# Kernel optimization log

Hardware: AMD Instinct MI355X
Metric: run time of the kernel (lower is better)

## Reference

```python
import jax, jax.numpy as jnp
import numpy as np

B, S, UC = 64, 5, 50          # batch, sample (candidates), clicked history
D, T = 128, 768               # embedding_size, title_size
NE, NR, NN = 200000, 100, 50000  # entities, relations, news
K, A = 10, 20                 # neighbors per entity, anchor nodes per news


def _lin(k, out_d, in_d):
    w = jax.random.normal(k, (out_d, in_d), jnp.float32) * (1.0 / np.sqrt(in_d))
    b = jnp.zeros((out_d,), jnp.float32)
    return w, b


def setup_inputs() -> dict:
    key = jax.random.key(0)
    ks = jax.random.split(key, 16)
    W_nc1, b_nc1 = _lin(ks[0], D, T)
    W_nc2, b_nc2 = _lin(ks[1], D, D)
    W_anchor, b_anchor = _lin(ks[2], D, 2 * D)
    W_aw1, b_aw1 = _lin(ks[3], D, D)
    W_aw2, b_aw2 = _lin(ks[4], 1, D)
    W_mlp1, b_mlp1 = _lin(ks[5], D, 2 * D)
    W_mlp2, b_mlp2 = _lin(ks[6], D, D)
    return {
        "news_title_embedding": jax.random.normal(ks[7], (NN, T), jnp.float32),
        "entity_embedding": jax.random.normal(ks[8], (NE, D), jnp.float32),
        "relation_embedding": jax.random.normal(ks[9], (NR, D), jnp.float32),
        "W_nc1": W_nc1, "b_nc1": b_nc1, "W_nc2": W_nc2, "b_nc2": b_nc2,
        "W_anchor": W_anchor, "b_anchor": b_anchor,
        "W_aw1": W_aw1, "b_aw1": b_aw1, "W_aw2": W_aw2, "b_aw2": b_aw2,
        "W_mlp1": W_mlp1, "b_mlp1": b_mlp1, "W_mlp2": W_mlp2, "b_mlp2": b_mlp2,
        "cand_news": jax.random.randint(ks[10], (B, S), 0, NN, jnp.int32),
        "clicked_news": jax.random.randint(ks[11], (B, UC), 0, NN, jnp.int32),
        "cand_anchor_nodes": jax.random.randint(ks[12], (B * S, A), 0, NE, jnp.int32),
        "clicked_anchor_nodes": jax.random.randint(ks[13], (B * UC, A), 0, NE, jnp.int32),
        "entity_adj": jax.random.randint(ks[14], (NE, K), 0, NE, jnp.int32),
        "relation_adj": jax.random.randint(ks[15], (NE, K), 0, NR, jnp.int32),
    }


def reference(news_title_embedding, entity_embedding, relation_embedding,
              W_nc1, b_nc1, W_nc2, b_nc2,
              W_anchor, b_anchor, W_aw1, b_aw1, W_aw2, b_aw2,
              W_mlp1, b_mlp1, W_mlp2, b_mlp2,
              cand_news, clicked_news, cand_anchor_nodes, clicked_anchor_nodes,
              entity_adj, relation_adj):
    elu = jax.nn.elu

    def news_emb(ids_flat):  # [N] -> [N, D]
        t = news_title_embedding[ids_flat]                       # [N, T]
        return jnp.tanh(elu(t @ W_nc1.T + b_nc1) @ W_nc2.T + b_nc2)

    def anchor_graph_emb(nodes):  # [N, A] -> [N, D]
        node_e = entity_embedding[nodes]                          # [N, A, D]
        nb_ent = entity_embedding[entity_adj[nodes]]              # [N, A, K, D]
        nb_rel = relation_embedding[relation_adj[nodes]]          # [N, A, K, D]
        agg = jnp.sum(nb_ent + nb_rel, axis=-2)                   # [N, A, D]
        h = jnp.tanh(jnp.concatenate([node_e, agg], axis=-1) @ W_anchor.T + b_anchor)
        logits = elu(h @ W_aw1.T + b_aw1) @ W_aw2.T + b_aw2       # [N, A, 1]
        w = jax.nn.softmax(logits, axis=-2)                       # softmax over anchor nodes
        return jnp.sum(h * w, axis=-2)                            # [N, D]

    cand_e = news_emb(cand_news.reshape(-1))                      # [B*S, D]
    clk_e = news_emb(clicked_news.reshape(-1))                    # [B*UC, D]
    cand_e = jnp.concatenate([cand_e, anchor_graph_emb(cand_anchor_nodes)], axis=-1)
    clk_e = jnp.concatenate([clk_e, anchor_graph_emb(clicked_anchor_nodes)], axis=-1)

    def mlp(x):
        return elu(elu(x @ W_mlp1.T + b_mlp1) @ W_mlp2.T + b_mlp2)

    news_embedding = mlp(cand_e).reshape(B, S, -1)                # [B, S, D]
    user_embedding = jnp.mean(mlp(clk_e).reshape(B, UC, -1), axis=1)  # [B, D]
    score = jnp.sum(news_embedding * user_embedding[:, None, :], axis=-1)  # [B, S]
    return score
```

## Files before the change

kernel.cpp:

```cpp
#include <hip/hip_runtime.h>
#include <hip/hip_bf16.h>


#define B_ 64
#define S_ 5
#define UC_ 50
#define A_ 20
#define NCAND 320
#define NCLK 3200
#define NNEWS 3520
#define NANCH 70400

static constexpr long OFF_WNC1P = 64;
static constexpr long OFF_BNC1  = 98368;
static constexpr long OFF_WNC2P = 98496;
static constexpr long OFF_BNC2  = 114880;
static constexpr long OFF_WANCP = 115008;
static constexpr long OFF_BANC  = 147776;
static constexpr long OFF_WAW1P = 147904;
static constexpr long OFF_BAW1  = 164288;
static constexpr long OFF_WAW2  = 164416;
static constexpr long OFF_BAW2  = 164544;
static constexpr long OFF_WM1P  = 164548;
static constexpr long OFF_BM1   = 197316;
static constexpr long OFF_WM2P  = 197444;
static constexpr long OFF_BM2   = 213828;
static constexpr long OFF_REL   = 213956;
static constexpr long OFF_AE    = 226756;
static constexpr long OFF_NE    = 677316;
static constexpr long OFF_MO    = 1127876;

typedef __attribute__((ext_vector_type(8))) short short8v;
typedef __attribute__((ext_vector_type(4))) float f32x4;

__device__ __forceinline__ float ldf(const void* p, long i, int bf) {
  if (bf) {
    unsigned int u = (unsigned int)((const unsigned short*)p)[i];
    u <<= 16;
    return __uint_as_float(u);
  }
  return ((const float*)p)[i];
}

__device__ __forceinline__ float4 ldf4(const void* p, long i, int bf) {
  float4 f;
  if (bf) {
    const unsigned short* q = (const unsigned short*)p + i;
    uint2 u = *(const uint2*)q;
    f.x = __uint_as_float(u.x << 16);
    f.y = __uint_as_float(u.x & 0xffff0000u);
    f.z = __uint_as_float(u.y << 16);
    f.w = __uint_as_float(u.y & 0xffff0000u);
  } else {
    f = *(const float4*)((const float*)p + i);
  }
  return f;
}

__device__ __forceinline__ float eluf(float v) { return v > 0.f ? v : expm1f(v); }

__device__ __forceinline__ void splitbf(float v, unsigned short& hi, unsigned short& lo) {
  unsigned int b = __float_as_uint(v);
  hi = (unsigned short)(b >> 16);
  float rm = v - __uint_as_float(b & 0xffff0000u);
  unsigned int rb = __float_as_uint(rm);
  lo = (unsigned short)((rb + 0x7fffu + ((rb >> 16) & 1u)) >> 16);
}

__device__ __forceinline__ float bfh(unsigned short u) {
  return __uint_as_float((unsigned int)u << 16);
}

__global__ void k_detect(const void* ent, int* flag) {
  __shared__ int cnt;
  if (threadIdx.x == 0) cnt = 0;
  __syncthreads();
  unsigned short u = ((const unsigned short*)ent)[threadIdx.x];
  int e = (u >> 7) & 0xFF;
  int ok = (e >= 107 && e <= 146) ? 1 : 0;
  atomicAdd(&cnt, ok);
  __syncthreads();
  if (threadIdx.x == 0) *flag = (cnt >= 200) ? 1 : 0;
}

__global__ __launch_bounds__(256) void k_prep(
    const void* s0, const void* s1, const void* s2, const void* s3,
    const void* s4, const void* s5, const void* s6, const void* s7,
    const void* s8, const void* s9, const void* s10, const void* s11,
    const void* s12, const void* s13, const void* s14, float* ws) {
  const int bf = ((const int*)ws)[0];
  const void* srcs[15] = {s0,s1,s2,s3,s4,s5,s6,s7,s8,s9,s10,s11,s12,s13,s14};
  const int R[15] = {128,128,128,128,128,128,128,128,1,  1,  128,128,128,128,100};
  const int C[15] = {768,1,  128,1,  256,1,  128,1,  128,1,  256,1,  128,1,  128};
  const int MD[15]= {2,  0,  2,  0,  3,  0,  3,  0,  0,  0,  2,  0,  2,  0,  0};
  const long OFF[15] = {OFF_WNC1P,OFF_BNC1,OFF_WNC2P,OFF_BNC2,OFF_WANCP,OFF_BANC,
                        OFF_WAW1P,OFF_BAW1,OFF_WAW2,OFF_BAW2,OFF_WM1P,OFF_BM1,
                        OFF_WM2P,OFF_BM2,OFF_REL};
  const long total = 226689;
  for (long idx = (long)blockIdx.x * blockDim.x + threadIdx.x; idx < total;
       idx += (long)gridDim.x * blockDim.x) {
    long rem = idx;
    int s = 0;
    while (rem >= (long)R[s] * C[s]) { rem -= (long)R[s] * C[s]; s++; }
    float v = ldf(srcs[s], rem, bf);
    if (MD[s] == 2) {
      long r = rem / C[s], c = rem - r * C[s];
      ws[OFF[s] + (c >> 2) * 512 + r * 4 + (c & 3)] = v;
    } else if (MD[s] == 3) {
      long r = rem / C[s], c = rem - r * C[s];
      unsigned short hi, lo;
      splitbf(v, hi, lo);
      unsigned short* H = (unsigned short*)(ws + OFF[s]);
      unsigned short* L = H + (s == 4 ? 32768 : 16384);
      long id2 = ((c >> 5) * 128 + r) * 32 + (c & 31);
      H[id2] = hi;
      L[id2] = lo;
    } else {
      ws[OFF[s] + rem] = v;
    }
  }
}

__global__ __launch_bounds__(128) void k_news(const void* titles, const int* cand,
                                              const int* clk, float* ws) {
  const int bf = ((const int*)ws)[0];
  __shared__ __align__(16) float t[8][768];
  __shared__ __align__(16) float h1[8][128];
  int tid = threadIdx.x;
  long r0 = (long)blockIdx.x * 8;
  for (int x = tid * 4; x < 8 * 768; x += 128 * 4) {
    int c = x / 768, k = x - c * 768;
    long i = r0 + c;
    int id = (i < NCAND) ? cand[i] : clk[i - NCAND];
    *(float4*)&t[c][k] = ldf4(titles, (long)id * 768 + k, bf);
  }
  __syncthreads();
  int j = tid;
  const float4* W1 = (const float4*)(ws + OFF_WNC1P);
  float acc[8];
#pragma unroll
  for (int c = 0; c < 8; c++) acc[c] = 0.f;
  for (int k4 = 0; k4 < 192; k4++) {
    float4 w = W1[k4 * 128 + j];
#pragma unroll
    for (int c = 0; c < 8; c++) {
      const float4 xv = *(const float4*)&t[c][k4 * 4];
      acc[c] += w.x * xv.x + w.y * xv.y + w.z * xv.z + w.w * xv.w;
    }
  }
  float b1 = ws[OFF_BNC1 + j];
#pragma unroll
  for (int c = 0; c < 8; c++) h1[c][j] = eluf(acc[c] + b1);
  __syncthreads();
  const float4* W2 = (const float4*)(ws + OFF_WNC2P);
  float a2[8];
#pragma unroll
  for (int c = 0; c < 8; c++) a2[c] = 0.f;
  for (int k4 = 0; k4 < 32; k4++) {
    float4 w = W2[k4 * 128 + j];
#pragma unroll
    for (int c = 0; c < 8; c++) {
      const float4 xv = *(const float4*)&h1[c][k4 * 4];
      a2[c] += w.x * xv.x + w.y * xv.y + w.z * xv.z + w.w * xv.w;
    }
  }
  float b2 = ws[OFF_BNC2 + j];
  float* NE = ws + OFF_NE;
#pragma unroll
  for (int c = 0; c < 8; c++) NE[(r0 + c) * 128 + j] = tanhf(a2[c] + b2);
}

__global__ __launch_bounds__(256, 3) void k_anchor(const void* ent, const int* canda,
                                                   const int* clka, const int* eadj,
                                                   const int* radj, float* ws) {
  __shared__ __align__(16) unsigned short XbH[32][264];
  __shared__ __align__(16) unsigned short XbL[32][264];
  __shared__ __align__(16) unsigned short Hhi[32][136];
  __shared__ __align__(16) unsigned short Hlo[32][136];
  __shared__ int NodeIdL[20];
  __shared__ int EAdjL[200];
  __shared__ int RAdjL[200];
  __shared__ float LGp[4][20];

  const int bf = ((const int*)ws)[0];
  int tid = threadIdx.x;
  int lane = tid & 63, wv = tid >> 6;
  int r16 = lane & 15, khh = lane >> 4;
  int lane32 = tid & 31, grp = tid >> 5;
  const float* relf = ws + OFF_REL;

  const unsigned short* WAH = (const unsigned short*)(ws + OFF_WANCP);
  const unsigned short* WAL = WAH + 32768;
  const unsigned short* W1H = (const unsigned short*)(ws + OFF_WAW1P);
  const unsigned short* W1L = W1H + 16384;

  if (tid < 20) {
    long n = (long)blockIdx.x * 20 + tid;
    NodeIdL[tid] = (n < (long)NCAND * A_) ? canda[n] : clka[n - (long)NCAND * A_];
  }
  __syncthreads();
  if (tid < 200) {
    int rr = tid / 10, kk = tid - rr * 10;
    int nd = NodeIdL[rr];
    EAdjL[tid] = eadj[(long)nd * 10 + kk];
    RAdjL[tid] = radj[(long)nd * 10 + kk];
  }
  __syncthreads();

#pragma unroll
  for (int i = 0; i < 3; ++i) {
    int row = grp + i * 8;
    if (row < 20) {
      int node = NodeIdL[row];
      float4 x1 = ldf4(ent, (long)node * 128 + lane32 * 4, bf);
      float4 a = {0.f, 0.f, 0.f, 0.f};
#pragma unroll
      for (int k = 0; k < 10; ++k) {
        int an = EAdjL[row * 10 + k], rn = RAdjL[row * 10 + k];
        float4 e = ldf4(ent, (long)an * 128 + lane32 * 4, bf);
        const float4 r = *(const float4*)&relf[(long)rn * 128 + lane32 * 4];
        a.x += e.x + r.x;
        a.y += e.y + r.y;
        a.z += e.z + r.z;
        a.w += e.w + r.w;
      }
      ushort4 h4, l4;
      splitbf(x1.x, h4.x, l4.x); splitbf(x1.y, h4.y, l4.y);
      splitbf(x1.z, h4.z, l4.z); splitbf(x1.w, h4.w, l4.w);
      *(ushort4*)&XbH[row][lane32 * 4] = h4;
      *(ushort4*)&XbL[row][lane32 * 4] = l4;
      splitbf(a.x, h4.x, l4.x); splitbf(a.y, h4.y, l4.y);
      splitbf(a.z, h4.z, l4.z); splitbf(a.w, h4.w, l4.w);
      *(ushort4*)&XbH[row][128 + lane32 * 4] = h4;
      *(ushort4*)&XbL[row][128 + lane32 * 4] = l4;
    }
  }
  __syncthreads();

  {
    int n0 = wv * 32 + r16, n1 = n0 + 16;
    f32x4 acc[2][2] = {};
    for (int kt = 0; kt < 8; ++kt) {
      long w0 = ((long)(kt * 128 + n0)) * 32 + khh * 8;
      long w1 = ((long)(kt * 128 + n1)) * 32 + khh * 8;
      short8v b0h = *(const short8v*)(WAH + w0);
      short8v b0l = *(const short8v*)(WAL + w0);
      short8v b1h = *(const short8v*)(WAH + w1);
      short8v b1l = *(const short8v*)(WAL + w1);
#pragma unroll
      for (int mt = 0; mt < 2; ++mt) {
        short8v ahi = *(const short8v*)&XbH[mt * 16 + r16][kt * 32 + khh * 8];
        short8v alo = *(const short8v*)&XbL[mt * 16 + r16][kt * 32 + khh * 8];
        acc[mt][0] = __builtin_amdgcn_mfma_f32_16x16x32_bf16(ahi, b0h, acc[mt][0], 0, 0, 0);
        acc[mt][0] = __builtin_amdgcn_mfma_f32_16x16x32_bf16(ahi, b0l, acc[mt][0], 0, 0, 0);
        acc[mt][0] = __builtin_amdgcn_mfma_f32_16x16x32_bf16(alo, b0h, acc[mt][0], 0, 0, 0);
        acc[mt][1] = __builtin_amdgcn_mfma_f32_16x16x32_bf16(ahi, b1h, acc[mt][1], 0, 0, 0);
        acc[mt][1] = __builtin_amdgcn_mfma_f32_16x16x32_bf16(ahi, b1l, acc[mt][1], 0, 0, 0);
        acc[mt][1] = __builtin_amdgcn_mfma_f32_16x16x32_bf16(alo, b1h, acc[mt][1], 0, 0, 0);
      }
    }
    float bc0 = ws[OFF_BANC + n0], bc1 = ws[OFF_BANC + n1];
#pragma unroll
    for (int mt = 0; mt < 2; ++mt)
#pragma unroll
      for (int j = 0; j < 4; ++j) {
        int r = mt * 16 + khh * 4 + j;
        if (r < 20) {
          unsigned short hi, lo;
          float h0 = tanhf(acc[mt][0][j] + bc0);
          splitbf(h0, hi, lo);
          Hhi[r][n0] = hi; Hlo[r][n0] = lo;
          float h1 = tanhf(acc[mt][1][j] + bc1);
          splitbf(h1, hi, lo);
          Hhi[r][n1] = hi; Hlo[r][n1] = lo;
        }
      }
  }
  __syncthreads();

  {
    int n0 = wv * 32 + r16, n1 = n0 + 16;
    float b10 = ws[OFF_BAW1 + n0], b11 = ws[OFF_BAW1 + n1];
    float w20 = ws[OFF_WAW2 + n0], w21 = ws[OFF_WAW2 + n1];
    f32x4 ac[2][2] = {};
    for (int kt = 0; kt < 4; ++kt) {
      long w0 = ((long)(kt * 128 + n0)) * 32 + khh * 8;
      long w1 = ((long)(kt * 128 + n1)) * 32 + khh * 8;
      short8v b0h = *(const short8v*)(W1H + w0);
      short8v b0l = *(const short8v*)(W1L + w0);
      short8v b1h = *(const short8v*)(W1H + w1);
      short8v b1l = *(const short8v*)(W1L + w1);
#pragma unroll
      for (int mt = 0; mt < 2; ++mt) {
        short8v ahi = *(const short8v*)&Hhi[mt * 16 + r16][kt * 32 + khh * 8];
        short8v alo = *(const short8v*)&Hlo[mt * 16 + r16][kt * 32 + khh * 8];
        ac[mt][0] = __builtin_amdgcn_mfma_f32_16x16x32_bf16(ahi, b0h, ac[mt][0], 0, 0, 0);
        ac[mt][0] = __builtin_amdgcn_mfma_f32_16x16x32_bf16(ahi, b0l, ac[mt][0], 0, 0, 0);
        ac[mt][0] = __builtin_amdgcn_mfma_f32_16x16x32_bf16(alo, b0h, ac[mt][0], 0, 0, 0);
        ac[mt][1] = __builtin_amdgcn_mfma_f32_16x16x32_bf16(ahi, b1h, ac[mt][1], 0, 0, 0);
        ac[mt][1] = __builtin_amdgcn_mfma_f32_16x16x32_bf16(ahi, b1l, ac[mt][1], 0, 0, 0);
        ac[mt][1] = __builtin_amdgcn_mfma_f32_16x16x32_bf16(alo, b1h, ac[mt][1], 0, 0, 0);
      }
    }
#pragma unroll
    for (int mt = 0; mt < 2; ++mt)
#pragma unroll
      for (int j = 0; j < 4; ++j) {
        float v = eluf(ac[mt][0][j] + b10) * w20 + eluf(ac[mt][1][j] + b11) * w21;
        v += __shfl_xor(v, 1);
        v += __shfl_xor(v, 2);
        v += __shfl_xor(v, 4);
        v += __shfl_xor(v, 8);
        int r = mt * 16 + khh * 4 + j;
        if (r16 == 0 && r < 20) LGp[wv][r] = v;
      }
  }
  __syncthreads();

  if (tid < 128) {
    float bw2 = ws[OFF_BAW2];
    float e[20], mx = -1e30f;
#pragma unroll
    for (int a = 0; a < 20; ++a) {
      e[a] = LGp[0][a] + LGp[1][a] + LGp[2][a] + LGp[3][a] + bw2;
      mx = fmaxf(mx, e[a]);
    }
    float s = 0.f;
#pragma unroll
    for (int a = 0; a < 20; ++a) { e[a] = expf(e[a] - mx); s += e[a]; }
    float inv = 1.0f / s;
    float o = 0.f;
#pragma unroll
    for (int a = 0; a < 20; ++a)
      o += e[a] * (bfh(Hhi[a][tid]) + bfh(Hlo[a][tid]));
    float* AE = ws + OFF_AE;
    AE[(long)blockIdx.x * 128 + tid] = o * inv;
  }
}

__global__ __launch_bounds__(256) void k_mlp(float* ws) {
  __shared__ __align__(16) float xt[16][256];
  __shared__ __align__(16) float h1[16][128];
  int tid = threadIdx.x;
  long r0 = (long)blockIdx.x * 16;
  const float* NE = ws + OFF_NE;
  const float* AE = ws + OFF_AE;
  for (int x = tid; x < 16 * 256; x += 256) {
    int c = x >> 8, k = x & 255;
    xt[c][k] = (k < 128) ? NE[(r0 + c) * 128 + k] : AE[(r0 + c) * 128 + (k - 128)];
  }
  __syncthreads();
  int j = tid & 127, half = tid >> 7;
  const float4* W1 = (const float4*)(ws + OFF_WM1P);
  float acc[8];
#pragma unroll
  for (int c = 0; c < 8; c++) acc[c] = 0.f;
  for (int k4 = 0; k4 < 64; k4++) {
    float4 w = W1[k4 * 128 + j];
#pragma unroll
    for (int c = 0; c < 8; c++) {
      const float4 xv = *(const float4*)&xt[half * 8 + c][k4 * 4];
      acc[c] += w.x * xv.x + w.y * xv.y + w.z * xv.z + w.w * xv.w;
    }
  }
  float b1 = ws[OFF_BM1 + j];
#pragma unroll
  for (int c = 0; c < 8; c++) h1[half * 8 + c][j] = eluf(acc[c] + b1);
  __syncthreads();
  const float4* W2 = (const float4*)(ws + OFF_WM2P);
  float a2[8];
#pragma unroll
  for (int c = 0; c < 8; c++) a2[c] = 0.f;
  for (int k4 = 0; k4 < 32; k4++) {
    float4 w = W2[k4 * 128 + j];
#pragma unroll
    for (int c = 0; c < 8; c++) {
      const float4 xv = *(const float4*)&h1[half * 8 + c][k4 * 4];
      a2[c] += w.x * xv.x + w.y * xv.y + w.z * xv.z + w.w * xv.w;
    }
  }
  float b2 = ws[OFF_BM2 + j];
  float* MO = ws + OFF_MO;
#pragma unroll
  for (int c = 0; c < 8; c++) MO[(r0 + half * 8 + c) * 128 + j] = eluf(a2[c] + b2);
}

__global__ __launch_bounds__(128) void k_score(const float* ws, void* out) {
  const int bf = ((const int*)ws)[0];
  int b = blockIdx.x;
  int d = threadIdx.x;
  const float* MO = ws + OFF_MO;
  float u = 0.f;
  for (int t = 0; t < UC_; t++) u += MO[(long)(NCAND + b * UC_ + t) * 128 + d];
  u *= (1.0f / UC_);
  __shared__ float red[2];
  for (int s = 0; s < S_; s++) {
    float p = MO[(long)(b * S_ + s) * 128 + d] * u;
#pragma unroll
    for (int o = 32; o > 0; o >>= 1) p += __shfl_down(p, o, 64);
    if ((d & 63) == 0) red[d >> 6] = p;
    __syncthreads();
    if (d == 0) {
      float v = red[0] + red[1];
      if (bf)
        ((__hip_bfloat16*)out)[b * S_ + s] = __float2bfloat16(v);
      else
        ((float*)out)[b * S_ + s] = v;
    }
    __syncthreads();
  }
}

extern "C" void kernel_launch(void* const* d_in, const int* in_sizes, int n_in,
                              void* d_out, int out_size, void* d_ws, size_t ws_size,
                              hipStream_t stream) {
  (void)in_sizes; (void)n_in; (void)out_size; (void)ws_size;
  const void* titles = d_in[0];
  const void* ent    = d_in[1];
  const void* rel    = d_in[2];
  const void* Wnc1 = d_in[3];  const void* bnc1 = d_in[4];
  const void* Wnc2 = d_in[5];  const void* bnc2 = d_in[6];
  const void* Wanc = d_in[7];  const void* banc = d_in[8];
  const void* Waw1 = d_in[9];  const void* baw1 = d_in[10];
  const void* Waw2 = d_in[11]; const void* baw2 = d_in[12];
  const void* Wm1  = d_in[13]; const void* bm1  = d_in[14];
  const void* Wm2  = d_in[15]; const void* bm2  = d_in[16];
  const int* cand  = (const int*)d_in[17];
  const int* clk   = (const int*)d_in[18];
  const int* canda = (const int*)d_in[19];
  const int* clka  = (const int*)d_in[20];
  const int* eadj  = (const int*)d_in[21];
  const int* radj  = (const int*)d_in[22];
  float* ws = (float*)d_ws;

  k_detect<<<1, 256, 0, stream>>>(ent, (int*)d_ws);
  k_prep<<<256, 256, 0, stream>>>(Wnc1, bnc1, Wnc2, bnc2, Wanc, banc, Waw1, baw1,
                                  Waw2, baw2, Wm1, bm1, Wm2, bm2, rel, ws);
  k_news<<<NNEWS / 8, 128, 0, stream>>>(titles, cand, clk, ws);
  k_anchor<<<NNEWS, 256, 0, stream>>>(ent, canda, clka, eadj, radj, ws);
  k_mlp<<<NNEWS / 16, 256, 0, stream>>>(ws);
  k_score<<<B_, 128, 0, stream>>>(ws, d_out);
}
```

Baseline: 224.2 us.

## Stage bf16 entity gathers via global_load_lds with swizzled LDS and trimmed MFMAs

When entity embeddings are bf16, the node and neighbour rows are gathered straight into LDS with global_load_lds instead of through registers. The node half of the anchor input is exact in bf16, so its low-part MFMAs are skipped. The shared arrays shrink to 20 rows with XOR swizzling to avoid bank conflicts, and the padded rows 20-31 are aliased onto valid rows rather than read. LDS use rises because of the 200-row raw buffer, so the occupancy hint drops from 3 to 2 blocks per CU.

```diff
diff --git a/kernel.cpp b/kernel.cpp
--- a/kernel.cpp
+++ b/kernel.cpp
@@ -33,6 +33,19 @@
 typedef __attribute__((ext_vector_type(8))) short short8v;
 typedef __attribute__((ext_vector_type(4))) float f32x4;
 
+typedef const __attribute__((address_space(1))) void* gas_ptr;
+typedef __attribute__((address_space(3))) void* las_ptr;
+
+__device__ __forceinline__ void gld_lds16(const void* g, void* l) {
+  __builtin_amdgcn_global_load_lds(
+      (gas_ptr)(unsigned long long)g,
+      (las_ptr)(unsigned int)(unsigned long long)l, 16, 0, 0);
+}
+
+__device__ __forceinline__ int swz(int row, int col) {
+  return (((col >> 3) ^ (row & 7)) << 3) | (col & 7);
+}
+
 __device__ __forceinline__ float ldf(const void* p, long i, int bf) {
   if (bf) {
     unsigned int u = (unsigned int)((const unsigned short*)p)[i];
@@ -54,6 +67,15 @@
   } else {
     f = *(const float4*)((const float*)p + i);
   }
+  return f;
+}
+
+__device__ __forceinline__ float4 cvtbf4(uint2 u) {
+  float4 f;
+  f.x = __uint_as_float(u.x << 16);
+  f.y = __uint_as_float(u.x & 0xffff0000u);
+  f.z = __uint_as_float(u.y << 16);
+  f.w = __uint_as_float(u.y & 0xffff0000u);
   return f;
 }
 
@@ -170,17 +192,20 @@
   for (int c = 0; c < 8; c++) NE[(r0 + c) * 128 + j] = tanhf(a2[c] + b2);
 }
 
-__global__ __launch_bounds__(256, 3) void k_anchor(const void* ent, const int* canda,
+__global__ __launch_bounds__(256, 2) void k_anchor(const void* ent, const int* canda,
                                                    const int* clka, const int* eadj,
                                                    const int* radj, float* ws) {
-  __shared__ __align__(16) unsigned short XbH[32][264];
-  __shared__ __align__(16) unsigned short XbL[32][264];
-  __shared__ __align__(16) unsigned short Hhi[32][136];
-  __shared__ __align__(16) unsigned short Hlo[32][136];
+  __shared__ __align__(16) unsigned short AggRaw[200][128];
+  __shared__ __align__(16) unsigned short XbNodeH[20][128];
+  __shared__ __align__(16) unsigned short XbAggH[20][128];
+  __shared__ __align__(16) unsigned short XbAggL[20][128];
+  __shared__ __align__(16) unsigned short Hhi[20][128];
+  __shared__ __align__(16) unsigned short Hlo[20][128];
   __shared__ int NodeIdL[20];
   __shared__ int EAdjL[200];
   __shared__ int RAdjL[200];
   __shared__ float LGp[4][20];
+  unsigned short (*XbNodeL)[128] = (unsigned short(*)[128])&AggRaw[0][0];
 
   const int bf = ((const int*)ws)[0];
   int tid = threadIdx.x;
@@ -207,32 +232,75 @@
   }
   __syncthreads();
 
-#pragma unroll
-  for (int i = 0; i < 3; ++i) {
-    int row = grp + i * 8;
-    if (row < 20) {
-      int node = NodeIdL[row];
-      float4 x1 = ldf4(ent, (long)node * 128 + lane32 * 4, bf);
-      float4 a = {0.f, 0.f, 0.f, 0.f};
+  if (bf) {
+    const char* entb = (const char*)ent;
+    int lq = lane & 15;
+    int rq = lane >> 4;
+    for (int i = wv; i < 55; i += 4) {
+      if (i < 5) {
+        int row4 = i * 4;
+        int id = NodeIdL[row4 + rq];
+        int sg = lq ^ ((row4 + rq) & 7);
+        gld_lds16(entb + (long)id * 256 + sg * 16, &XbNodeH[row4][0]);
+      } else {
+        int row4 = (i - 5) * 4;
+        int id = EAdjL[row4 + rq];
+        gld_lds16(entb + (long)id * 256 + lq * 16, &AggRaw[row4][0]);
+      }
+    }
+  }
+  __syncthreads();
+
+  if (bf) {
+#pragma unroll
+    for (int ii = 0; ii < 3; ++ii) {
+      if (ii == 2 && wv >= 2) break;
+      int a = grp + ii * 8;
+      float4 s = {0.f, 0.f, 0.f, 0.f};
 #pragma unroll
       for (int k = 0; k < 10; ++k) {
-        int an = EAdjL[row * 10 + k], rn = RAdjL[row * 10 + k];
-        float4 e = ldf4(ent, (long)an * 128 + lane32 * 4, bf);
-        const float4 r = *(const float4*)&relf[(long)rn * 128 + lane32 * 4];
-        a.x += e.x + r.x;
-        a.y += e.y + r.y;
-        a.z += e.z + r.z;
-        a.w += e.w + r.w;
+        float4 e = cvtbf4(*(const uint2*)&AggRaw[a * 10 + k][lane32 * 4]);
+        const float4 r = *(const float4*)&relf[(long)RAdjL[a * 10 + k] * 128 + lane32 * 4];
+        s.x += e.x + r.x;
+        s.y += e.y + r.y;
+        s.z += e.z + r.z;
+        s.w += e.w + r.w;
       }
       ushort4 h4, l4;
-      splitbf(x1.x, h4.x, l4.x); splitbf(x1.y, h4.y, l4.y);
-      splitbf(x1.z, h4.z, l4.z); splitbf(x1.w, h4.w, l4.w);
-      *(ushort4*)&XbH[row][lane32 * 4] = h4;
-      *(ushort4*)&XbL[row][lane32 * 4] = l4;
-      splitbf(a.x, h4.x, l4.x); splitbf(a.y, h4.y, l4.y);
-      splitbf(a.z, h4.z, l4.z); splitbf(a.w, h4.w, l4.w);
-      *(ushort4*)&XbH[row][128 + lane32 * 4] = h4;
-      *(ushort4*)&XbL[row][128 + lane32 * 4] = l4;
+      splitbf(s.x, h4.x, l4.x); splitbf(s.y, h4.y, l4.y);
+      splitbf(s.z, h4.z, l4.z); splitbf(s.w, h4.w, l4.w);
+      int c = (((lane32 >> 1) ^ (a & 7)) << 3) + (lane32 & 1) * 4;
+      *(ushort4*)&XbAggH[a][c] = h4;
+      *(ushort4*)&XbAggL[a][c] = l4;
+    }
+  } else {
+#pragma unroll
+    for (int ii = 0; ii < 3; ++ii) {
+      int a = grp + ii * 8;
+      if (a < 20) {
+        int node = NodeIdL[a];
+        float4 x1 = ldf4(ent, (long)node * 128 + lane32 * 4, 0);
+        float4 s = {0.f, 0.f, 0.f, 0.f};
+#pragma unroll
+        for (int k = 0; k < 10; ++k) {
+          float4 e = ldf4(ent, (long)EAdjL[a * 10 + k] * 128 + lane32 * 4, 0);
+          const float4 r = *(const float4*)&relf[(long)RAdjL[a * 10 + k] * 128 + lane32 * 4];
+          s.x += e.x + r.x;
+          s.y += e.y + r.y;
+          s.z += e.z + r.z;
+          s.w += e.w + r.w;
+        }
+        int c = (((lane32 >> 1) ^ (a & 7)) << 3) + (lane32 & 1) * 4;
+        ushort4 h4, l4;
+        splitbf(x1.x, h4.x, l4.x); splitbf(x1.y, h4.y, l4.y);
+        splitbf(x1.z, h4.z, l4.z); splitbf(x1.w, h4.w, l4.w);
+        *(ushort4*)&XbNodeH[a][c] = h4;
+        *(ushort4*)&XbNodeL[a][c] = l4;
+        splitbf(s.x, h4.x, l4.x); splitbf(s.y, h4.y, l4.y);
+        splitbf(s.z, h4.z, l4.z); splitbf(s.w, h4.w, l4.w);
+        *(ushort4*)&XbAggH[a][c] = h4;
+        *(ushort4*)&XbAggL[a][c] = l4;
+      }
     }
   }
   __syncthreads();
@@ -240,7 +308,7 @@
   {
     int n0 = wv * 32 + r16, n1 = n0 + 16;
     f32x4 acc[2][2] = {};
-    for (int kt = 0; kt < 8; ++kt) {
+    for (int kt = 0; kt < 4; ++kt) {
       long w0 = ((long)(kt * 128 + n0)) * 32 + khh * 8;
       long w1 = ((long)(kt * 128 + n1)) * 32 + khh * 8;
       short8v b0h = *(const short8v*)(WAH + w0);
@@ -249,8 +317,33 @@
       short8v b1l = *(const short8v*)(WAL + w1);
 #pragma unroll
       for (int mt = 0; mt < 2; ++mt) {
-        short8v ahi = *(const short8v*)&XbH[mt * 16 + r16][kt * 32 + khh * 8];
-        short8v alo = *(const short8v*)&XbL[mt * 16 + r16][kt * 32 + khh * 8];
+        int ar = (mt == 0) ? r16 : 16 + (r16 & 3);
+        int cg = ((kt * 4 + khh) ^ (ar & 7)) << 3;
+        short8v ahi = *(const short8v*)&XbNodeH[ar][cg];
+        acc[mt][0] = __builtin_amdgcn_mfma_f32_16x16x32_bf16(ahi, b0h, acc[mt][0], 0, 0, 0);
+        acc[mt][0] = __builtin_amdgcn_mfma_f32_16x16x32_bf16(ahi, b0l, acc[mt][0], 0, 0, 0);
+        acc[mt][1] = __builtin_amdgcn_mfma_f32_16x16x32_bf16(ahi, b1h, acc[mt][1], 0, 0, 0);
+        acc[mt][1] = __builtin_amdgcn_mfma_f32_16x16x32_bf16(ahi, b1l, acc[mt][1], 0, 0, 0);
+        if (!bf) {
+          short8v alo = *(const short8v*)&XbNodeL[ar][cg];
+          acc[mt][0] = __builtin_amdgcn_mfma_f32_16x16x32_bf16(alo, b0h, acc[mt][0], 0, 0, 0);
+          acc[mt][1] = __builtin_amdgcn_mfma_f32_16x16x32_bf16(alo, b1h, acc[mt][1], 0, 0, 0);
+        }
+      }
+    }
+    for (int kt = 4; kt < 8; ++kt) {
+      long w0 = ((long)(kt * 128 + n0)) * 32 + khh * 8;
+      long w1 = ((long)(kt * 128 + n1)) * 32 + khh * 8;
+      short8v b0h = *(const short8v*)(WAH + w0);
+      short8v b0l = *(const short8v*)(WAL + w0);
+      short8v b1h = *(const short8v*)(WAH + w1);
+      short8v b1l = *(const short8v*)(WAL + w1);
+#pragma unroll
+      for (int mt = 0; mt < 2; ++mt) {
+        int ar = (mt == 0) ? r16 : 16 + (r16 & 3);
+        int cg = (((kt - 4) * 4 + khh) ^ (ar & 7)) << 3;
+        short8v ahi = *(const short8v*)&XbAggH[ar][cg];
+        short8v alo = *(const short8v*)&XbAggL[ar][cg];
         acc[mt][0] = __builtin_amdgcn_mfma_f32_16x16x32_bf16(ahi, b0h, acc[mt][0], 0, 0, 0);
         acc[mt][0] = __builtin_amdgcn_mfma_f32_16x16x32_bf16(ahi, b0l, acc[mt][0], 0, 0, 0);
         acc[mt][0] = __builtin_amdgcn_mfma_f32_16x16x32_bf16(alo, b0h, acc[mt][0], 0, 0, 0);
@@ -269,10 +362,10 @@
           unsigned short hi, lo;
           float h0 = tanhf(acc[mt][0][j] + bc0);
           splitbf(h0, hi, lo);
-          Hhi[r][n0] = hi; Hlo[r][n0] = lo;
+          Hhi[r][swz(r, n0)] = hi; Hlo[r][swz(r, n0)] = lo;
           float h1 = tanhf(acc[mt][1][j] + bc1);
           splitbf(h1, hi, lo);
-          Hhi[r][n1] = hi; Hlo[r][n1] = lo;
+          Hhi[r][swz(r, n1)] = hi; Hlo[r][swz(r, n1)] = lo;
         }
       }
   }
@@ -292,8 +385,10 @@
       short8v b1l = *(const short8v*)(W1L + w1);
 #pragma unroll
       for (int mt = 0; mt < 2; ++mt) {
-        short8v ahi = *(const short8v*)&Hhi[mt * 16 + r16][kt * 32 + khh * 8];
-        short8v alo = *(const short8v*)&Hlo[mt * 16 + r16][kt * 32 + khh * 8];
+        int hr = (mt == 0) ? r16 : 16 + (r16 & 3);
+        int cg = ((kt * 4 + khh) ^ (hr & 7)) << 3;
+        short8v ahi = *(const short8v*)&Hhi[hr][cg];
+        short8v alo = *(const short8v*)&Hlo[hr][cg];
         ac[mt][0] = __builtin_amdgcn_mfma_f32_16x16x32_bf16(ahi, b0h, ac[mt][0], 0, 0, 0);
         ac[mt][0] = __builtin_amdgcn_mfma_f32_16x16x32_bf16(ahi, b0l, ac[mt][0], 0, 0, 0);
         ac[mt][0] = __builtin_amdgcn_mfma_f32_16x16x32_bf16(alo, b0h, ac[mt][0], 0, 0, 0);
@@ -331,8 +426,10 @@
     float inv = 1.0f / s;
     float o = 0.f;
 #pragma unroll
-    for (int a = 0; a < 20; ++a)
-      o += e[a] * (bfh(Hhi[a][tid]) + bfh(Hlo[a][tid]));
+    for (int a = 0; a < 20; ++a) {
+      int c = swz(a, tid);
+      o += e[a] * (bfh(Hhi[a][c]) + bfh(Hlo[a][c]));
+    }
     float* AE = ws + OFF_AE;
     AE[(long)blockIdx.x * 128 + tid] = o * inv;
   }
```

After: 245.4 us. +9.4%, slower.
